# Kernel tuning notes

Measured on AMD Instinct MI355X. Metric: run time of the kernel, lower is better.

Reference implementation:

```python
import jax, jax.numpy as jnp
import numpy as np

N_NODES = 20000
N_EDGES = 320000
F_IN = 4
PERIODS = 12
OUT_CH = 256   # A3TGCN out_channels (hard-coded in TemporalGNN)
HID = 128      # linear1 hidden
OUT_DIM = 12


def setup_inputs() -> dict:
    key = jax.random.key(0)
    ks = jax.random.split(key, 24)
    s = 0.1
    inp = {
        "x": jax.random.normal(ks[0], (N_NODES, F_IN, PERIODS), jnp.float32),
        "edge_index": jax.random.randint(ks[1], (2, N_EDGES), 0, N_NODES, dtype=jnp.int64),
        "edge_attr": jax.random.uniform(ks[2], (N_EDGES,), jnp.float32),
        # A3TGCN attention over periods
        "attention": jax.random.uniform(ks[3], (PERIODS,), jnp.float32),
        # TGCN: three GCNConv(in=F_IN, out=OUT_CH) weights+biases (z, r, h gates)
        "Wz": jax.random.normal(ks[4], (F_IN, OUT_CH), jnp.float32) * s,
        "bz": jnp.zeros((OUT_CH,), jnp.float32),
        "Wr": jax.random.normal(ks[5], (F_IN, OUT_CH), jnp.float32) * s,
        "br": jnp.zeros((OUT_CH,), jnp.float32),
        "Wh": jax.random.normal(ks[6], (F_IN, OUT_CH), jnp.float32) * s,
        "bh": jnp.zeros((OUT_CH,), jnp.float32),
        # TGCN: three Linear(2*OUT_CH -> OUT_CH) for the gates
        "Lzw": jax.random.normal(ks[7], (2 * OUT_CH, OUT_CH), jnp.float32) * s,
        "Lzb": jnp.zeros((OUT_CH,), jnp.float32),
        "Lrw": jax.random.normal(ks[8], (2 * OUT_CH, OUT_CH), jnp.float32) * s,
        "Lrb": jnp.zeros((OUT_CH,), jnp.float32),
        "Lhw": jax.random.normal(ks[9], (2 * OUT_CH, OUT_CH), jnp.float32) * s,
        "Lhb": jnp.zeros((OUT_CH,), jnp.float32),
        # MLP head
        "W1": jax.random.normal(ks[10], (OUT_CH, HID), jnp.float32) * s,
        "b1": jnp.zeros((HID,), jnp.float32),
        "W2": jax.random.normal(ks[11], (HID, OUT_DIM), jnp.float32) * s,
        "b2": jnp.zeros((OUT_DIM,), jnp.float32),
    }
    return inp


def _forward(x, edge_index, edge_attr, attention,
             Wz, bz, Wr, br, Wh, bh,
             Lzw, Lzb, Lrw, Lrb, Lhw, Lhb,
             W1, b1, W2, b2):
    N, F, T = x.shape
    src, dst = edge_index[0], edge_index[1]
    # GCN normalization with self-loops (PyG gcn_norm, fill_value=1):
    loop = jnp.arange(N)
    src_a = jnp.concatenate([src, loop])
    dst_a = jnp.concatenate([dst, loop])
    w_a = jnp.concatenate([edge_attr, jnp.ones((N,), x.dtype)])
    deg = jax.ops.segment_sum(w_a, dst_a, num_segments=N)
    dinv = jnp.where(deg > 0, jax.lax.rsqrt(deg), 0.0)
    norm = dinv[src_a] * w_a * dinv[dst_a]  # [E+N]

    def gcn(xt, W, b):
        xw = xt @ W                                   # [N, OUT_CH]
        msg = norm[:, None] * xw[src_a]               # [E+N, OUT_CH] (memory-bound gather)
        return jax.ops.segment_sum(msg, dst_a, num_segments=N) + b

    Hzero = jnp.zeros((N, OUT_CH), x.dtype)  # A3TGCN uses H=None -> zeros each period
    probs = jax.nn.softmax(attention)
    H_accum = jnp.zeros((N, OUT_CH), x.dtype)
    for t in range(T):  # fixed small number of periods
        xt = x[:, :, t]
        Z = jax.nn.sigmoid(jnp.concatenate([gcn(xt, Wz, bz), Hzero], axis=1) @ Lzw + Lzb)
        R = jax.nn.sigmoid(jnp.concatenate([gcn(xt, Wr, br), Hzero], axis=1) @ Lrw + Lrb)
        Htil = jnp.tanh(jnp.concatenate([gcn(xt, Wh, bh), Hzero * R], axis=1) @ Lhw + Lhb)
        Hnew = Z * Hzero + (1.0 - Z) * Htil
        H_accum = H_accum + probs[t] * Hnew

    out_hidden = H_accum
    h = jax.nn.relu(H_accum)
    h = jax.nn.relu(h @ W1 + b1)
    h = h @ W2 + b2
    return h, out_hidden


def reference(x, edge_index, edge_attr, attention,
              Wz, bz, Wr, br, Wh, bh,
              Lzw, Lzb, Lrw, Lrb, Lhw, Lhb,
              W1, b1, W2, b2):
    return _forward(x, edge_index, edge_attr, attention,
                    Wz, bz, Wr, br, Wh, bh,
                    Lzw, Lzb, Lrw, Lrb, Lhw, Lhb,
                    W1, b1, W2, b2)
```

## Files before the change

kernel.cpp:

```cpp
#include <hip/hip_runtime.h>
#include <math.h>

#define NN 20000
#define NE 320000
#define TP 12
#define OC 256
#define HIDN 128
#define OD 12
#define FT 48
#define CAP 64
#define NPB 16
#define LOG2E 1.44269504088896340736f

#define NB_E    ((NE + 255) / 256)
#define NB_XT   ((NN * TP + 255) / 256)
#define NB_DINV ((NN + 255) / 256)

#define OFF_CNT    0
#define OFF_DEG    (OFF_CNT + NN)
#define OFF_DINV   (OFF_DEG + NN)
#define OFF_MZ     (OFF_DINV + NN)
#define OFF_MH     (OFF_MZ + 4*OC)
#define OFF_CZ     (OFF_MH + 4*OC)
#define OFF_CH     (OFF_CZ + OC)
#define OFF_PROBS  (OFF_CH + OC)
#define OFF_W2T    (OFF_PROBS + 16)
#define OFF_ELL    (OFF_W2T + HIDN*OD)
#define OFF_P      (OFF_ELL + 2*NN*CAP)
#define OFF_XT     (OFF_P + NN*FT)
#define NEED_ELL   ((size_t)(OFF_XT) * 4)
#define NEED_XT    ((size_t)(OFF_XT + NN*FT) * 4)

__device__ __forceinline__ int detect64(const void* ei) {
    const unsigned long long* p = (const unsigned long long*)ei;
    unsigned long long v = p[threadIdx.x & 63];
    return (__ballot(v < (unsigned long long)NN) == ~0ull) ? 1 : 0;
}

__device__ __forceinline__ int load_idx(const void* ei, int is64, long off) {
    return is64 ? (int)((const long long*)ei)[off] : ((const int*)ei)[off];
}

__global__ __launch_bounds__(256) void build_kernel(
    const void* ei, const float* __restrict__ w, const float* __restrict__ x,
    int* __restrict__ cnt, float* __restrict__ deg, float2* __restrict__ ell,
    float4* __restrict__ XT4, int useELL, int useXT) {
    int bid = blockIdx.x;
    if (bid < NB_E) {
        int is64 = detect64(ei);
        int e = bid * 256 + threadIdx.x;
        if (e < NE) {
            int src = load_idx(ei, is64, e);
            int dst = load_idx(ei, is64, (long)NE + e);
            float we = w[e];
            atomicAdd(&deg[dst], we);
            if (useELL) {
                int slot = atomicAdd(&cnt[dst], 1);
                if (slot < CAP)
                    ell[dst * CAP + slot] = make_float2(__int_as_float(src), we);
            }
        }
    } else if (useXT) {
        int idx = (bid - NB_E) * 256 + threadIdx.x;
        if (idx < NN * TP) {
            int n = idx / TP;
            int t = idx - n * TP;
            const float* xb = x + n * FT + t;
            XT4[idx] = make_float4(xb[0], xb[12], xb[24], xb[36]);
        }
    }
}

__global__ __launch_bounds__(256) void prep_kernel(
    const float* __restrict__ deg, float* __restrict__ dinv,
    const float* __restrict__ Wz, const float* __restrict__ bz,
    const float* __restrict__ Wh, const float* __restrict__ bh,
    const float* __restrict__ Lzw, const float* __restrict__ Lzb,
    const float* __restrict__ Lhw, const float* __restrict__ Lhb,
    const float* __restrict__ att, const float* __restrict__ W2,
    float* __restrict__ Mz, float* __restrict__ Mh,
    float* __restrict__ cz, float* __restrict__ ch,
    float* __restrict__ probs, float* __restrict__ W2T, float4* __restrict__ XT4) {
    int bid = blockIdx.x;
    int tid = threadIdx.x;
    if (bid < NB_DINV) {
        int n = bid * 256 + tid;
        if (n < NN) dinv[n] = 1.0f / sqrtf(deg[n] + 1.0f);
    } else if (bid == NB_DINV) {
        int c = tid;
        float az0 = 0, az1 = 0, az2 = 0, az3 = 0, abz = 0;
        float ah0 = 0, ah1 = 0, ah2 = 0, ah3 = 0, abh = 0;
        for (int k = 0; k < OC; ++k) {
            float lz = Lzw[k * OC + c];
            float lh = Lhw[k * OC + c];
            az0 += Wz[k] * lz;
            az1 += Wz[OC + k] * lz;
            az2 += Wz[2 * OC + k] * lz;
            az3 += Wz[3 * OC + k] * lz;
            abz += bz[k] * lz;
            ah0 += Wh[k] * lh;
            ah1 += Wh[OC + k] * lh;
            ah2 += Wh[2 * OC + k] * lh;
            ah3 += Wh[3 * OC + k] * lh;
            abh += bh[k] * lh;
        }
        const float sz = LOG2E, sh2 = 2.0f * LOG2E;
        Mz[c] = az0 * sz; Mz[OC + c] = az1 * sz; Mz[2 * OC + c] = az2 * sz; Mz[3 * OC + c] = az3 * sz;
        Mh[c] = ah0 * sh2; Mh[OC + c] = ah1 * sh2; Mh[2 * OC + c] = ah2 * sh2; Mh[3 * OC + c] = ah3 * sh2;
        cz[c] = (abz + Lzb[c]) * sz;
        ch[c] = (abh + Lhb[c]) * sh2;
        if (c == 0) {
            float m = att[0];
            for (int t = 1; t < TP; ++t) m = fmaxf(m, att[t]);
            float sum = 0.0f, e[TP];
            for (int t = 0; t < TP; ++t) { e[t] = expf(att[t] - m); sum += e[t]; }
            for (int t = 0; t < TP; ++t) probs[t] = e[t] / sum;
        }
    } else if (bid == NB_DINV + 1) {
        if (tid < HIDN)
            for (int k = 0; k < OD; ++k) W2T[k * HIDN + tid] = W2[tid * OD + k];
    } else {
        int idx = (bid - (NB_DINV + 2)) * 256 + tid;
        if (idx < NN * TP) {
            int n = idx / TP;
            float dn = 1.0f / sqrtf(deg[n] + 1.0f);
            float4 v = XT4[idx];
            XT4[idx] = make_float4(dn * v.x, dn * v.y, dn * v.z, dn * v.w);
        }
    }
}

__global__ __launch_bounds__(256) void gather_kernel(
    const int* __restrict__ cnt, const float* __restrict__ dinv,
    const float2* __restrict__ ell, const float4* __restrict__ XT4,
    const float* __restrict__ x, int useXT, float4* __restrict__ P4) {
    int idx = blockIdx.x * 256 + threadIdx.x;
    int q = idx & 1;
    int i = idx >> 1;
    int n = i / TP;
    int t = i - n * TP;
    float4 acc = make_float4(0.f, 0.f, 0.f, 0.f);
    if (q == 0) {
        if (useXT) acc = XT4[n * TP + t];
        else {
            const float* xb = x + n * FT + t;
            float dn = dinv[n];
            acc = make_float4(dn * xb[0], dn * xb[12], dn * xb[24], dn * xb[36]);
        }
    }
    int cn = cnt[n];
    cn = cn < CAP ? cn : CAP;
    for (int e = q; e < cn; e += 2) {
        float2 r = ell[n * CAP + e];
        int s = __float_as_int(r.x);
        float4 xs;
        float wv = r.y;
        if (useXT) xs = XT4[s * TP + t];
        else {
            const float* xb = x + s * FT + t;
            xs = make_float4(xb[0], xb[12], xb[24], xb[36]);
            wv *= dinv[s];
        }
        acc.x = fmaf(wv, xs.x, acc.x);
        acc.y = fmaf(wv, xs.y, acc.y);
        acc.z = fmaf(wv, xs.z, acc.z);
        acc.w = fmaf(wv, xs.w, acc.w);
    }
    acc.x += __shfl_xor(acc.x, 1);
    acc.y += __shfl_xor(acc.y, 1);
    acc.z += __shfl_xor(acc.z, 1);
    acc.w += __shfl_xor(acc.w, 1);
    if (q == 0) {
        float dn = dinv[n];
        P4[i] = make_float4(dn * acc.x, dn * acc.y, dn * acc.z, dn * acc.w);
    }
}

__global__ __launch_bounds__(256) void initP_kernel(
    const float* __restrict__ x, const float* __restrict__ dinv, float4* __restrict__ P4) {
    int idx = blockIdx.x * 256 + threadIdx.x;
    if (idx >= NN * TP) return;
    int n = idx / TP;
    int t = idx - n * TP;
    const float* xb = x + n * FT + t;
    float dn = dinv[n], s = dn * dn;
    P4[idx] = make_float4(s * xb[0], s * xb[12], s * xb[24], s * xb[36]);
}

__global__ __launch_bounds__(256) void scatterB_kernel(
    const void* ei, const float* __restrict__ w, const float* __restrict__ dinv,
    const float* __restrict__ x, float* __restrict__ P) {
    int idx = blockIdx.x * 256 + threadIdx.x;
    if (idx >= NE * FT) return;
    int is64 = detect64(ei);
    int e = idx / FT;
    int k = idx - e * FT;
    int src = load_idx(ei, is64, e);
    int dst = load_idx(ei, is64, (long)NE + e);
    float nrm = dinv[src] * w[e] * dinv[dst];
    int t = k >> 2, f = k & 3;
    atomicAdd(&P[dst * FT + k], nrm * x[src * FT + f * TP + t]);
}

__global__ __launch_bounds__(512, 8) void fused_kernel(
    const float4* __restrict__ P4,
    const float* __restrict__ Mz, const float* __restrict__ Mh,
    const float* __restrict__ cz, const float* __restrict__ chv,
    const float* __restrict__ probs,
    const float* __restrict__ W1, const float* __restrict__ b1,
    const float* __restrict__ W2T, const float* __restrict__ b2,
    float* __restrict__ out) {
    int c = threadIdx.x;
    int ch = c & (OC - 1);
    int half = c >> 8;
    int nb = blockIdx.x * NPB;
    __shared__ float4 shp4[NPB * TP];
    __shared__ float shh[NPB][OC];
    __shared__ float shh1[NPB][HIDN + 4];

    if (c < NPB * TP) shp4[c] = P4[nb * TP + c];
    float mz0 = Mz[ch], mz1 = Mz[OC + ch], mz2 = Mz[2 * OC + ch], mz3 = Mz[3 * OC + ch];
    float mh0 = Mh[ch], mh1 = Mh[OC + ch], mh2 = Mh[2 * OC + ch], mh3 = Mh[3 * OC + ch];
    float czc = cz[ch], chc = chv[ch];
    float pr[TP];
#pragma unroll
    for (int t = 0; t < TP; ++t) pr[t] = probs[t];
    __syncthreads();

    int m0 = half * 8;
#pragma unroll 2
    for (int mm = 0; mm < 8; ++mm) {
        int m = m0 + mm;
        float ha = 0.0f, hb = 0.0f;
#pragma unroll
        for (int t = 0; t < TP; t += 2) {
#pragma unroll
            for (int u = 0; u < 2; ++u) {
                float4 p = shp4[m * TP + t + u];
                float az = czc, ah = chc;
                az = fmaf(p.x, mz0, az); ah = fmaf(p.x, mh0, ah);
                az = fmaf(p.y, mz1, az); ah = fmaf(p.y, mh1, ah);
                az = fmaf(p.z, mz2, az); ah = fmaf(p.z, mh2, ah);
                az = fmaf(p.w, mz3, az); ah = fmaf(p.w, mh3, ah);
                float ea = __builtin_exp2f(az);
                float eb = __builtin_exp2f(ah);
                float den = (1.0f + ea) * (1.0f + eb);
                float num = pr[t + u] * (eb - 1.0f);
                float v = num * __builtin_amdgcn_rcpf(den);
                if (u == 0) ha += v; else hb += v;
            }
        }
        float hacc = ha + hb;
        out[NN * OD + (nb + m) * OC + ch] = hacc;
        shh[m][ch] = fmaxf(hacc, 0.0f);
    }
    __syncthreads();

    {
        int j = c & (HIDN - 1);
        int mq = (c >> 7) * 4;
        float s0 = 0, s1 = 0, s2 = 0, s3 = 0;
        for (int k4 = 0; k4 < OC / 4; ++k4) {
            int kb = k4 * 4;
            float w0 = W1[(kb + 0) * HIDN + j];
            float w1 = W1[(kb + 1) * HIDN + j];
            float w2 = W1[(kb + 2) * HIDN + j];
            float w3 = W1[(kb + 3) * HIDN + j];
            float4 h0 = *(const float4*)&shh[mq + 0][kb];
            float4 h1 = *(const float4*)&shh[mq + 1][kb];
            float4 h2 = *(const float4*)&shh[mq + 2][kb];
            float4 h3 = *(const float4*)&shh[mq + 3][kb];
            s0 = fmaf(w0, h0.x, fmaf(w1, h0.y, fmaf(w2, h0.z, fmaf(w3, h0.w, s0))));
            s1 = fmaf(w0, h1.x, fmaf(w1, h1.y, fmaf(w2, h1.z, fmaf(w3, h1.w, s1))));
            s2 = fmaf(w0, h2.x, fmaf(w1, h2.y, fmaf(w2, h2.z, fmaf(w3, h2.w, s2))));
            s3 = fmaf(w0, h3.x, fmaf(w1, h3.y, fmaf(w2, h3.z, fmaf(w3, h3.w, s3))));
        }
        float bb = b1[j];
        shh1[mq + 0][j] = fmaxf(s0 + bb, 0.0f);
        shh1[mq + 1][j] = fmaxf(s1 + bb, 0.0f);
        shh1[mq + 2][j] = fmaxf(s2 + bb, 0.0f);
        shh1[mq + 3][j] = fmaxf(s3 + bb, 0.0f);
    }
    __syncthreads();

    if (c < NPB * OD) {
        int m = c / OD;
        int k = c - m * OD;
        const float4* w2r = (const float4*)&W2T[k * HIDN];
        const float4* hr  = (const float4*)&shh1[m][0];
        float a = b2[k];
        for (int j4 = 0; j4 < HIDN / 4; ++j4) {
            float4 w = w2r[j4];
            float4 h = hr[j4];
            a = fmaf(w.x, h.x, fmaf(w.y, h.y, fmaf(w.z, h.z, fmaf(w.w, h.w, a))));
        }
        out[(nb + m) * OD + k] = a;
    }
}

extern "C" void kernel_launch(void* const* d_in, const int* in_sizes, int n_in,
                              void* d_out, int out_size, void* d_ws, size_t ws_size,
                              hipStream_t stream) {
    const float* x   = (const float*)d_in[0];
    const void*  ei  = d_in[1];
    const float* ea  = (const float*)d_in[2];
    const float* att = (const float*)d_in[3];
    const float* Wz  = (const float*)d_in[4];
    const float* bz  = (const float*)d_in[5];
    const float* Wh  = (const float*)d_in[8];
    const float* bh  = (const float*)d_in[9];
    const float* Lzw = (const float*)d_in[10];
    const float* Lzb = (const float*)d_in[11];
    const float* Lhw = (const float*)d_in[14];
    const float* Lhb = (const float*)d_in[15];
    const float* W1  = (const float*)d_in[16];
    const float* b1  = (const float*)d_in[17];
    const float* W2  = (const float*)d_in[18];
    const float* b2  = (const float*)d_in[19];

    float* out = (float*)d_out;
    float* ws  = (float*)d_ws;

    int*    cnt   = (int*)(ws + OFF_CNT);
    float*  deg   = ws + OFF_DEG;
    float*  dinv  = ws + OFF_DINV;
    float*  Mz    = ws + OFF_MZ;
    float*  Mh    = ws + OFF_MH;
    float*  cz    = ws + OFF_CZ;
    float*  ch    = ws + OFF_CH;
    float*  probs = ws + OFF_PROBS;
    float*  W2T   = ws + OFF_W2T;
    float2* ell   = (float2*)(ws + OFF_ELL);
    float*  XT    = ws + OFF_XT;

    int useELL = (ws_size >= NEED_ELL) ? 1 : 0;
    int useXT  = (ws_size >= NEED_XT) ? 1 : 0;
    float* P = useELL ? (ws + OFF_P) : (ws + OFF_ELL);

    hipMemsetAsync(ws, 0, (size_t)OFF_DINV * sizeof(float), stream);
    build_kernel<<<NB_E + (useXT ? NB_XT : 0), 256, 0, stream>>>(
        ei, ea, x, cnt, deg, ell, (float4*)XT, useELL, useXT);
    prep_kernel<<<NB_DINV + 2 + (useXT ? NB_XT : 0), 256, 0, stream>>>(
        deg, dinv, Wz, bz, Wh, bh, Lzw, Lzb, Lhw, Lhb, att, W2,
        Mz, Mh, cz, ch, probs, W2T, (float4*)XT);
    if (useELL) {
        gather_kernel<<<2 * NN * TP / 256, 256, 0, stream>>>(
            cnt, dinv, ell, (const float4*)XT, x, useXT, (float4*)P);
    } else {
        initP_kernel<<<(NN * TP + 255) / 256, 256, 0, stream>>>(x, dinv, (float4*)P);
        scatterB_kernel<<<(NE * FT + 255) / 256, 256, 0, stream>>>(ei, ea, dinv, x, P);
    }
    fused_kernel<<<NN / NPB, 512, 0, stream>>>((const float4*)P, Mz, Mh, cz, ch, probs,
                                               W1, b1, W2T, b2, out);
}
```

Before: 168.2 us.

## Pair gate reciprocals across timesteps and retile the hidden-layer matvec

The gate loop now handles two nodes at a time and merges the two per-timestep fractions into one, computing one reciprocal per pair of timesteps instead of one per timestep. The exp arguments are clamped to avoid overflow in the combined denominator. The first MLP layer is retiled so each thread computes a 2x2 block (two nodes by two hidden units) using float2 weight loads rather than four nodes by one unit. This trades fewer rcp instructions for extra multiplies and clamps, and may change register pressure.

```diff
diff --git a/kernel.cpp b/kernel.cpp
--- a/kernel.cpp
+++ b/kernel.cpp
@@ -202,6 +202,23 @@
     atomicAdd(&P[dst * FT + k], nrm * x[src * FT + f * TP + t]);
 }
 
+__device__ __forceinline__ void gate_unit(float4 p, float mz0, float mz1, float mz2,
+                                          float mz3, float mh0, float mh1, float mh2,
+                                          float mh3, float czc, float chc, float prt,
+                                          float& num, float& den) {
+    float az = czc, ah = chc;
+    az = fmaf(p.x, mz0, az); ah = fmaf(p.x, mh0, ah);
+    az = fmaf(p.y, mz1, az); ah = fmaf(p.y, mh1, ah);
+    az = fmaf(p.z, mz2, az); ah = fmaf(p.z, mh2, ah);
+    az = fmaf(p.w, mz3, az); ah = fmaf(p.w, mh3, ah);
+    az = fminf(fmaxf(az, -20.0f), 20.0f);
+    ah = fminf(fmaxf(ah, -20.0f), 20.0f);
+    float ea = __builtin_exp2f(az);
+    float eb = __builtin_exp2f(ah);
+    den = (1.0f + ea) * (1.0f + eb);
+    num = prt * (eb - 1.0f);
+}
+
 __global__ __launch_bounds__(512, 8) void fused_kernel(
     const float4* __restrict__ P4,
     const float* __restrict__ Mz, const float* __restrict__ Mh,
@@ -227,59 +244,59 @@
     for (int t = 0; t < TP; ++t) pr[t] = probs[t];
     __syncthreads();
 
-    int m0 = half * 8;
-#pragma unroll 2
-    for (int mm = 0; mm < 8; ++mm) {
-        int m = m0 + mm;
-        float ha = 0.0f, hb = 0.0f;
+    int m0g = half * 8;
+#pragma unroll
+    for (int mm = 0; mm < 8; mm += 2) {
+        int ma = m0g + mm;
+        int mb = ma + 1;
+        float acc_a = 0.0f, acc_b = 0.0f;
 #pragma unroll
         for (int t = 0; t < TP; t += 2) {
-#pragma unroll
-            for (int u = 0; u < 2; ++u) {
-                float4 p = shp4[m * TP + t + u];
-                float az = czc, ah = chc;
-                az = fmaf(p.x, mz0, az); ah = fmaf(p.x, mh0, ah);
-                az = fmaf(p.y, mz1, az); ah = fmaf(p.y, mh1, ah);
-                az = fmaf(p.z, mz2, az); ah = fmaf(p.z, mh2, ah);
-                az = fmaf(p.w, mz3, az); ah = fmaf(p.w, mh3, ah);
-                float ea = __builtin_exp2f(az);
-                float eb = __builtin_exp2f(ah);
-                float den = (1.0f + ea) * (1.0f + eb);
-                float num = pr[t + u] * (eb - 1.0f);
-                float v = num * __builtin_amdgcn_rcpf(den);
-                if (u == 0) ha += v; else hb += v;
-            }
-        }
-        float hacc = ha + hb;
-        out[NN * OD + (nb + m) * OC + ch] = hacc;
-        shh[m][ch] = fmaxf(hacc, 0.0f);
+            float na0, da0, na1, da1, nb0, db0, nb1, db1;
+            gate_unit(shp4[ma * TP + t],     mz0, mz1, mz2, mz3, mh0, mh1, mh2, mh3,
+                      czc, chc, pr[t],     na0, da0);
+            gate_unit(shp4[ma * TP + t + 1], mz0, mz1, mz2, mz3, mh0, mh1, mh2, mh3,
+                      czc, chc, pr[t + 1], na1, da1);
+            gate_unit(shp4[mb * TP + t],     mz0, mz1, mz2, mz3, mh0, mh1, mh2, mh3,
+                      czc, chc, pr[t],     nb0, db0);
+            gate_unit(shp4[mb * TP + t + 1], mz0, mz1, mz2, mz3, mh0, mh1, mh2, mh3,
+                      czc, chc, pr[t + 1], nb1, db1);
+            float cra = fmaf(na1, da0, na0 * da1);
+            float crb = fmaf(nb1, db0, nb0 * db1);
+            acc_a = fmaf(cra, __builtin_amdgcn_rcpf(da0 * da1), acc_a);
+            acc_b = fmaf(crb, __builtin_amdgcn_rcpf(db0 * db1), acc_b);
+        }
+        out[NN * OD + (nb + ma) * OC + ch] = acc_a;
+        out[NN * OD + (nb + mb) * OC + ch] = acc_b;
+        shh[ma][ch] = fmaxf(acc_a, 0.0f);
+        shh[mb][ch] = fmaxf(acc_b, 0.0f);
     }
     __syncthreads();
 
     {
-        int j = c & (HIDN - 1);
-        int mq = (c >> 7) * 4;
-        float s0 = 0, s1 = 0, s2 = 0, s3 = 0;
+        int jp = c & 63;
+        int mp = c >> 6;
+        int j0 = jp * 2;
+        int m0 = mp * 2;
+        float s0x = 0, s0y = 0, s1x = 0, s1y = 0;
         for (int k4 = 0; k4 < OC / 4; ++k4) {
             int kb = k4 * 4;
-            float w0 = W1[(kb + 0) * HIDN + j];
-            float w1 = W1[(kb + 1) * HIDN + j];
-            float w2 = W1[(kb + 2) * HIDN + j];
-            float w3 = W1[(kb + 3) * HIDN + j];
-            float4 h0 = *(const float4*)&shh[mq + 0][kb];
-            float4 h1 = *(const float4*)&shh[mq + 1][kb];
-            float4 h2 = *(const float4*)&shh[mq + 2][kb];
-            float4 h3 = *(const float4*)&shh[mq + 3][kb];
-            s0 = fmaf(w0, h0.x, fmaf(w1, h0.y, fmaf(w2, h0.z, fmaf(w3, h0.w, s0))));
-            s1 = fmaf(w0, h1.x, fmaf(w1, h1.y, fmaf(w2, h1.z, fmaf(w3, h1.w, s1))));
-            s2 = fmaf(w0, h2.x, fmaf(w1, h2.y, fmaf(w2, h2.z, fmaf(w3, h2.w, s2))));
-            s3 = fmaf(w0, h3.x, fmaf(w1, h3.y, fmaf(w2, h3.z, fmaf(w3, h3.w, s3))));
-        }
-        float bb = b1[j];
-        shh1[mq + 0][j] = fmaxf(s0 + bb, 0.0f);
-        shh1[mq + 1][j] = fmaxf(s1 + bb, 0.0f);
-        shh1[mq + 2][j] = fmaxf(s2 + bb, 0.0f);
-        shh1[mq + 3][j] = fmaxf(s3 + bb, 0.0f);
+            float4 h0 = *(const float4*)&shh[m0 + 0][kb];
+            float4 h1 = *(const float4*)&shh[m0 + 1][kb];
+            float2 wA = *(const float2*)&W1[(kb + 0) * HIDN + j0];
+            float2 wB = *(const float2*)&W1[(kb + 1) * HIDN + j0];
+            float2 wC = *(const float2*)&W1[(kb + 2) * HIDN + j0];
+            float2 wD = *(const float2*)&W1[(kb + 3) * HIDN + j0];
+            s0x = fmaf(h0.x, wA.x, fmaf(h0.y, wB.x, fmaf(h0.z, wC.x, fmaf(h0.w, wD.x, s0x))));
+            s0y = fmaf(h0.x, wA.y, fmaf(h0.y, wB.y, fmaf(h0.z, wC.y, fmaf(h0.w, wD.y, s0y))));
+            s1x = fmaf(h1.x, wA.x, fmaf(h1.y, wB.x, fmaf(h1.z, wC.x, fmaf(h1.w, wD.x, s1x))));
+            s1y = fmaf(h1.x, wA.y, fmaf(h1.y, wB.y, fmaf(h1.z, wC.y, fmaf(h1.w, wD.y, s1y))));
+        }
+        float2 bb = *(const float2*)&b1[j0];
+        *(float2*)&shh1[m0 + 0][j0] = make_float2(fmaxf(s0x + bb.x, 0.0f),
+                                                  fmaxf(s0y + bb.y, 0.0f));
+        *(float2*)&shh1[m0 + 1][j0] = make_float2(fmaxf(s1x + bb.x, 0.0f),
+                                                  fmaxf(s1y + bb.y, 0.0f));
     }
     __syncthreads();
 
```

Result: slower. 200.1 us (+19.0%).
